# Kernel optimization log

Hardware: AMD Instinct MI355X
Metric: run time of the kernel (lower is better)

The kernel has to match this reference:

```python
import jax, jax.numpy as jnp
import numpy as np

VLAD_K = 8   # vlad_cluster
GHOST_K = 2  # ghost_cluster
IN_DIM = 512
EPS = 1e-12  # F.normalize eps


def setup_inputs() -> dict:
    key = jax.random.key(0)
    k1, k2, k3, k4 = jax.random.split(key, 4)
    N, C, H, W = 32, IN_DIM, 16, 64
    KG = VLAD_K + GHOST_K
    x = jax.random.normal(k1, (N, C, H, W), dtype=jnp.float32)
    # 1x1 conv weight [KG, C, 1, 1] -> store as [KG, C]; bias [KG]
    conv_w = jax.random.normal(k2, (KG, C), dtype=jnp.float32) * (1.0 / np.sqrt(C))
    conv_b = jax.random.normal(k3, (KG,), dtype=jnp.float32) * 0.01
    centers = jax.random.uniform(k4, (KG, C), dtype=jnp.float32)
    return {"x": x, "conv_w": conv_w, "conv_b": conv_b, "centers": centers}


def reference(x, conv_w, conv_b, centers):
    N, C, H, W = x.shape
    P = H * W
    xf = x.reshape(N, C, P)                                   # [N,C,P]
    # 1x1 conv == per-position matmul over channels
    logits = jnp.einsum('ncp,kc->nkp', xf, conv_w) + conv_b[None, :, None]
    a = jax.nn.softmax(logits, axis=1)                        # softmax over clusters, [N,KG,P]
    # algebraic rewrite of sum_p a*(x - c): (a @ x^T) - (sum_p a) * c
    ax = jnp.einsum('nkp,ncp->nkc', a, xf)                    # [N,KG,C]
    a_sum = a.sum(axis=-1)                                    # [N,KG]
    cluster_res = ax - a_sum[..., None] * centers[None]       # [N,KG,C]
    cluster_res = cluster_res[:, :VLAD_K, :]                  # drop ghost clusters
    norm = jnp.linalg.norm(cluster_res, axis=-1, keepdims=True)
    cluster_res = cluster_res / jnp.maximum(norm, EPS)        # L2 normalize per cluster
    return cluster_res.reshape(N, VLAD_K * C)
```

## Files before the change

kernel.cpp:

```cpp
#include <hip/hip_runtime.h>
#include <math.h>

#define N_    32
#define C_    512
#define P_    1024
#define KG_   10
#define KV_   8
#define PBLK_ 64
#define NPB_  (P_ / PBLK_)
#define PS_   81

__global__ __launch_bounds__(512) void vlad_fused(
    const float* __restrict__ x, const float* __restrict__ w,
    const float* __restrict__ bias, float* __restrict__ ax_ws,
    float* __restrict__ asum_blk) {
  __shared__ float part[PBLK_ * PS_];
  __shared__ float a_lds[KV_][64];
  const int t  = threadIdx.x;
  const int pl = t & 63;
  const int cg = __builtin_amdgcn_readfirstlane(threadIdx.x >> 6);
  const int n  = blockIdx.x >> 4;
  const int pb = blockIdx.x & 15;
  const int p0 = pb * PBLK_;

  const float* xp = x + ((size_t)n * C_ + cg * 64) * P_ + p0 + pl;

  float acc[KG_];
#pragma unroll
  for (int k = 0; k < KG_; ++k) acc[k] = 0.f;

#pragma unroll 8
  for (int i = 0; i < 64; ++i) {
    const float xv = xp[(size_t)i * P_];
    const int c = cg * 64 + i;
#pragma unroll
    for (int k = 0; k < KG_; ++k) acc[k] += xv * w[k * C_ + c];
  }

#pragma unroll
  for (int k = 0; k < KG_; ++k) part[pl * PS_ + cg * KG_ + k] = acc[k];
  __syncthreads();

  if (t < 64) {
    float l[KG_];
    float m = -1e30f;
#pragma unroll
    for (int k = 0; k < KG_; ++k) {
      float s = bias[k];
#pragma unroll
      for (int g = 0; g < 8; ++g) s += part[t * PS_ + g * KG_ + k];
      l[k] = s;
      m = fmaxf(m, s);
    }
    float sum = 0.f;
#pragma unroll
    for (int k = 0; k < KG_; ++k) { l[k] = __expf(l[k] - m); sum += l[k]; }
    const float inv = 1.f / sum;
#pragma unroll
    for (int k = 0; k < KV_; ++k) {
      const float a = l[k] * inv;
      a_lds[k][t] = a;
      float s = a;
      s += __shfl_xor(s, 1, 64);  s += __shfl_xor(s, 2, 64);
      s += __shfl_xor(s, 4, 64);  s += __shfl_xor(s, 8, 64);
      s += __shfl_xor(s, 16, 64); s += __shfl_xor(s, 32, 64);
      if (t == 0) asum_blk[(n * NPB_ + pb) * KV_ + k] = s;
    }
  }
  __syncthreads();

  float ak[KV_];
#pragma unroll
  for (int k = 0; k < KV_; ++k) ak[k] = a_lds[k][pl];

  const float* xq = x + (size_t)n * C_ * P_ + p0 + pl;
  float* axn = ax_ws + (size_t)n * KV_ * C_;

  const bool h1 = pl & 1, h2 = pl & 2, h4 = pl & 4, h8 = pl & 8, h16 = pl & 16;
  const int o = ((pl & 1) << 4) | ((pl & 2) << 2) | (pl & 4)
              | (((pl >> 3) & 1) << 1) | ((pl >> 4) & 1);
  const int occ = o >> 3;
  const int ok  = o & 7;

#pragma unroll 2
  for (int q = 0; q < 16; ++q) {
    const int c0 = cg * 64 + q * 4;
    float v[32];
#pragma unroll
    for (int cc = 0; cc < 4; ++cc) {
      const float xv = xq[(size_t)(c0 + cc) * P_];
#pragma unroll
      for (int k = 0; k < 8; ++k) v[cc * 8 + k] = xv * ak[k];
    }

#pragma unroll
    for (int j = 0; j < 16; ++j) {
      float send = h1 ? v[j] : v[j + 16];
      float keep = h1 ? v[j + 16] : v[j];
      v[j] = keep + __shfl_xor(send, 1, 64);
    }
#pragma unroll
    for (int j = 0; j < 8; ++j) {
      float send = h2 ? v[j] : v[j + 8];
      float keep = h2 ? v[j + 8] : v[j];
      v[j] = keep + __shfl_xor(send, 2, 64);
    }
#pragma unroll
    for (int j = 0; j < 4; ++j) {
      float send = h4 ? v[j] : v[j + 4];
      float keep = h4 ? v[j + 4] : v[j];
      v[j] = keep + __shfl_xor(send, 4, 64);
    }
#pragma unroll
    for (int j = 0; j < 2; ++j) {
      float send = h8 ? v[j] : v[j + 2];
      float keep = h8 ? v[j + 2] : v[j];
      v[j] = keep + __shfl_xor(send, 8, 64);
    }
    {
      float send = h16 ? v[0] : v[1];
      float keep = h16 ? v[1] : v[0];
      v[0] = keep + __shfl_xor(send, 16, 64);
    }
    v[0] += __shfl_xor(v[0], 32, 64);

    if (pl < 32)
      atomicAdd(&axn[ok * C_ + c0 + occ], v[0]);
  }
}

__global__ __launch_bounds__(256) void vlad_fin(
    const float* __restrict__ ax_ws, const float* __restrict__ asum_blk,
    const float* __restrict__ centers, float* __restrict__ out) {
  __shared__ float sred[4];
  const int n = blockIdx.x >> 3;
  const int k = blockIdx.x & 7;
  const int t = threadIdx.x, lane = t & 63, wv = t >> 6;

  float asv = 0.f;
#pragma unroll
  for (int pb = 0; pb < NPB_; ++pb)
    asv += asum_blk[(n * NPB_ + pb) * KV_ + k];

  const int c = t * 2;
  const float2 av = *reinterpret_cast<const float2*>(&ax_ws[((size_t)n * KV_ + k) * C_ + c]);
  const float2 ct = *reinterpret_cast<const float2*>(&centers[k * C_ + c]);
  const float r0 = av.x - asv * ct.x;
  const float r1 = av.y - asv * ct.y;

  float ss = r0 * r0 + r1 * r1;
#pragma unroll
  for (int d = 1; d < 64; d <<= 1) ss += __shfl_xor(ss, d, 64);
  if (lane == 0) sred[wv] = ss;
  __syncthreads();
  const float tot = (sred[0] + sred[1]) + (sred[2] + sred[3]);
  const float inv = 1.f / fmaxf(sqrtf(tot), 1e-12f);

  out[(size_t)n * (KV_ * C_) + k * C_ + c]     = r0 * inv;
  out[(size_t)n * (KV_ * C_) + k * C_ + c + 1] = r1 * inv;
}

extern "C" void kernel_launch(void* const* d_in, const int* in_sizes, int n_in,
                              void* d_out, int out_size, void* d_ws, size_t ws_size,
                              hipStream_t stream) {
  const float* x       = (const float*)d_in[0];
  const float* conv_w  = (const float*)d_in[1];
  const float* conv_b  = (const float*)d_in[2];
  const float* centers = (const float*)d_in[3];
  float* out = (float*)d_out;

  float* ax_ws    = (float*)d_ws;
  float* asum_blk = ax_ws + (size_t)N_ * KV_ * C_;

  hipMemsetAsync(ax_ws, 0, (size_t)N_ * KV_ * C_ * sizeof(float), stream);
  hipLaunchKernelGGL(vlad_fused, dim3(N_ * NPB_), dim3(512), 0, stream,
                     x, conv_w, conv_b, ax_ws, asum_blk);
  hipLaunchKernelGGL(vlad_fin,   dim3(N_ * KV_),  dim3(256), 0, stream,
                     ax_ws, asum_blk, centers, out);
}
```

Before: 132.0 us.

## Process two positions per thread and replace atomics with per-block partials

Doubles the position block to 128 so each thread loads a float2 and handles two spatial positions in both the logits pass and the aggregation pass. This halves the shuffle-based butterfly reductions per unit of data. The global atomicAdd accumulation into ax is replaced by plain stores of per-block partial sums, which also removes the memset. The finalize kernel now sums 8 partials per element. The grid drops to 256 blocks of 512 threads, which lowers occupancy and latency hiding, and the workspace grows.

```diff
diff --git a/kernel.cpp b/kernel.cpp
--- a/kernel.cpp
+++ b/kernel.cpp
@@ -6,42 +6,50 @@
 #define P_    1024
 #define KG_   10
 #define KV_   8
-#define PBLK_ 64
+#define PBLK_ 128
 #define NPB_  (P_ / PBLK_)
+#define NSB_  16
 #define PS_   81
 
 __global__ __launch_bounds__(512) void vlad_fused(
     const float* __restrict__ x, const float* __restrict__ w,
-    const float* __restrict__ bias, float* __restrict__ ax_ws,
+    const float* __restrict__ bias, float* __restrict__ ax_part,
     float* __restrict__ asum_blk) {
   __shared__ float part[PBLK_ * PS_];
-  __shared__ float a_lds[KV_][64];
+  __shared__ float a_lds[KV_][PBLK_];
   const int t  = threadIdx.x;
   const int pl = t & 63;
   const int cg = __builtin_amdgcn_readfirstlane(threadIdx.x >> 6);
-  const int n  = blockIdx.x >> 4;
-  const int pb = blockIdx.x & 15;
+  const int n  = blockIdx.x >> 3;
+  const int pb = blockIdx.x & 7;
   const int p0 = pb * PBLK_;
 
-  const float* xp = x + ((size_t)n * C_ + cg * 64) * P_ + p0 + pl;
-
-  float acc[KG_];
-#pragma unroll
-  for (int k = 0; k < KG_; ++k) acc[k] = 0.f;
+  const float* xp = x + ((size_t)n * C_ + cg * 64) * P_ + p0 + 2 * pl;
+
+  float l0[KG_], l1[KG_];
+#pragma unroll
+  for (int k = 0; k < KG_; ++k) { l0[k] = 0.f; l1[k] = 0.f; }
 
 #pragma unroll 8
   for (int i = 0; i < 64; ++i) {
-    const float xv = xp[(size_t)i * P_];
+    const float2 xv = *reinterpret_cast<const float2*>(&xp[(size_t)i * P_]);
     const int c = cg * 64 + i;
 #pragma unroll
-    for (int k = 0; k < KG_; ++k) acc[k] += xv * w[k * C_ + c];
-  }
-
-#pragma unroll
-  for (int k = 0; k < KG_; ++k) part[pl * PS_ + cg * KG_ + k] = acc[k];
+    for (int k = 0; k < KG_; ++k) {
+      const float wk = w[k * C_ + c];
+      l0[k] += xv.x * wk;
+      l1[k] += xv.y * wk;
+    }
+  }
+
+#pragma unroll
+  for (int k = 0; k < KG_; ++k) part[pl * PS_ + cg * KG_ + k] = l0[k];
+#pragma unroll
+  for (int k = 0; k < KG_; ++k) part[(64 + pl) * PS_ + cg * KG_ + k] = l1[k];
   __syncthreads();
 
-  if (t < 64) {
+  if (t < 128) {
+    const int wv = t >> 6;
     float l[KG_];
     float m = -1e30f;
 #pragma unroll
@@ -64,17 +72,21 @@
       s += __shfl_xor(s, 1, 64);  s += __shfl_xor(s, 2, 64);
       s += __shfl_xor(s, 4, 64);  s += __shfl_xor(s, 8, 64);
       s += __shfl_xor(s, 16, 64); s += __shfl_xor(s, 32, 64);
-      if (t == 0) asum_blk[(n * NPB_ + pb) * KV_ + k] = s;
+      if ((t & 63) == 0)
+        asum_blk[((size_t)n * NSB_ + pb * 2 + wv) * KV_ + k] = s;
     }
   }
   __syncthreads();
 
-  float ak[KV_];
-#pragma unroll
-  for (int k = 0; k < KV_; ++k) ak[k] = a_lds[k][pl];
-
-  const float* xq = x + (size_t)n * C_ * P_ + p0 + pl;
-  float* axn = ax_ws + (size_t)n * KV_ * C_;
+  float ak0[KV_], ak1[KV_];
+#pragma unroll
+  for (int k = 0; k < KV_; ++k) {
+    ak0[k] = a_lds[k][pl];
+    ak1[k] = a_lds[k][64 + pl];
+  }
+
+  const float* xq = x + (size_t)n * C_ * P_ + p0 + 2 * pl;
+  float* axp = ax_part + ((size_t)n * NPB_ + pb) * KV_ * C_;
 
   const bool h1 = pl & 1, h2 = pl & 2, h4 = pl & 4, h8 = pl & 8, h16 = pl & 16;
   const int o = ((pl & 1) << 4) | ((pl & 2) << 2) | (pl & 4)
@@ -88,9 +100,10 @@
     float v[32];
 #pragma unroll
     for (int cc = 0; cc < 4; ++cc) {
-      const float xv = xq[(size_t)(c0 + cc) * P_];
-#pragma unroll
-      for (int k = 0; k < 8; ++k) v[cc * 8 + k] = xv * ak[k];
+      const float2 xv = *reinterpret_cast<const float2*>(&xq[(size_t)(c0 + cc) * P_]);
+#pragma unroll
+      for (int k = 0; k < 8; ++k)
+        v[cc * 8 + k] = xv.x * ak0[k] + xv.y * ak1[k];
     }
 
 #pragma unroll
@@ -125,12 +138,12 @@
     v[0] += __shfl_xor(v[0], 32, 64);
 
     if (pl < 32)
-      atomicAdd(&axn[ok * C_ + c0 + occ], v[0]);
+      axp[ok * C_ + c0 + occ] = v[0];
   }
 }
 
 __global__ __launch_bounds__(256) void vlad_fin(
-    const float* __restrict__ ax_ws, const float* __restrict__ asum_blk,
+    const float* __restrict__ ax_part, const float* __restrict__ asum_blk,
     const float* __restrict__ centers, float* __restrict__ out) {
   __shared__ float sred[4];
   const int n = blockIdx.x >> 3;
@@ -139,14 +152,22 @@
 
   float asv = 0.f;
 #pragma unroll
-  for (int pb = 0; pb < NPB_; ++pb)
-    asv += asum_blk[(n * NPB_ + pb) * KV_ + k];
+  for (int s = 0; s < NSB_; ++s)
+    asv += asum_blk[((size_t)n * NSB_ + s) * KV_ + k];
 
   const int c = t * 2;
-  const float2 av = *reinterpret_cast<const float2*>(&ax_ws[((size_t)n * KV_ + k) * C_ + c]);
+  float ax0 = 0.f, ax1 = 0.f;
+#pragma unroll
+  for (int pb = 0; pb < NPB_; ++pb) {
+    const float2 av = *reinterpret_cast<const float2*>(
+        &ax_part[(((size_t)n * NPB_ + pb) * KV_ + k) * C_ + c]);
+    ax0 += av.x;
+    ax1 += av.y;
+  }
+
   const float2 ct = *reinterpret_cast<const float2*>(&centers[k * C_ + c]);
-  const float r0 = av.x - asv * ct.x;
-  const float r1 = av.y - asv * ct.y;
+  const float r0 = ax0 - asv * ct.x;
+  const float r1 = ax1 - asv * ct.y;
 
   float ss = r0 * r0 + r1 * r1;
 #pragma unroll
@@ -169,12 +190,11 @@
   const float* centers = (const float*)d_in[3];
   float* out = (float*)d_out;
 
-  float* ax_ws    = (float*)d_ws;
-  float* asum_blk = ax_ws + (size_t)N_ * KV_ * C_;
-
-  hipMemsetAsync(ax_ws, 0, (size_t)N_ * KV_ * C_ * sizeof(float), stream);
+  float* ax_part  = (float*)d_ws;
+  float* asum_blk = ax_part + (size_t)N_ * NPB_ * KV_ * C_;
+
   hipLaunchKernelGGL(vlad_fused, dim3(N_ * NPB_), dim3(512), 0, stream,
-                     x, conv_w, conv_b, ax_ws, asum_blk);
+                     x, conv_w, conv_b, ax_part, asum_blk);
   hipLaunchKernelGGL(vlad_fin,   dim3(N_ * KV_),  dim3(256), 0, stream,
-                     ax_ws, asum_blk, centers, out);
+                     ax_part, asum_blk, centers, out);
 }
```

Result: faster. 123.2 us (-6.6%).
